# Performance work log

Hardware: AMD Instinct MI355X
Metric: run time of the kernel (lower is better)

The kernel has to match this reference:

```python
import jax, jax.numpy as jnp
import numpy as np

B, C, D, H, W = 4, 256, 16, 16, 16


def setup_inputs() -> dict:
    key = jax.random.key(0)
    ks = jax.random.split(key, 9)
    s = 1.0 / np.sqrt(C)
    inp = {
        "x": jax.random.normal(ks[0], (B, C, D, H, W), dtype=jnp.float32),
        "wq": jax.random.normal(ks[1], (C, C), dtype=jnp.float32) * s,
        "bq": jax.random.normal(ks[2], (C,), dtype=jnp.float32) * 0.02,
        "wk": jax.random.normal(ks[3], (C, C), dtype=jnp.float32) * s,
        "bk": jax.random.normal(ks[4], (C,), dtype=jnp.float32) * 0.02,
        "wv": jax.random.normal(ks[5], (C, C), dtype=jnp.float32) * s,
        "bv": jax.random.normal(ks[6], (C,), dtype=jnp.float32) * 0.02,
        "wp": jax.random.normal(ks[7], (C, C), dtype=jnp.float32) * s,
        "bp": jax.random.normal(ks[8], (C,), dtype=jnp.float32) * 0.02,
    }
    return inp


def reference(x, wq, bq, wk, bk, wv, bv, wp, bp):
    b, c, d, h, w = x.shape
    xf = x.reshape(b, c, d * h * w)  # (B, C, N)
    # 1x1 Conv3d == per-voxel linear map over channels
    q = jnp.einsum('oc,bcn->bon', wq, xf) + bq[:, None]
    k = jnp.einsum('oc,bcn->bon', wk, xf) + bk[:, None]
    v = jnp.einsum('oc,bcn->bon', wv, xf) + bv[:, None]
    # scores[b,i,j] = q[:, :, i] . k[:, :, j], scaled AFTER the bmm (as in source)
    scores = jnp.einsum('bci,bcj->bij', q, k) * (c ** -0.5)
    p = jax.nn.softmax(scores, axis=2)  # (B, N, N), softmax over keys j
    # attention[b,c,i] = sum_j v[b,c,j] * p[b,i,j]
    attn = jnp.einsum('bcj,bij->bci', v, p)
    out = jnp.einsum('oc,bcn->bon', wp, attn) + bp[:, None]
    return x + out.reshape(b, c, d, h, w)
```

## Files before the change

kernel.cpp:

```cpp
#include <hip/hip_runtime.h>

typedef unsigned short u16;
typedef unsigned int u32;
typedef __bf16 v8bf __attribute__((ext_vector_type(8)));
typedef float v4f __attribute__((ext_vector_type(4)));

#define DEV __device__ __forceinline__

constexpr int CB = 4;
constexpr int C = 256;
constexpr int NN = 4096;
constexpr float LOG2E = 1.4426950408889634f;
constexpr int PST = 44;

DEV u16 f2bf(float f) {
  union { float f; u32 u; } v; v.f = f;
  u32 r = v.u + 0x7fffu + ((v.u >> 16) & 1u);
  return (u16)(r >> 16);
}
DEV float bf2f(u16 h) {
  union { u32 u; float f; } v; v.u = ((u32)h) << 16; return v.f;
}

DEV void dma16(const u16* g, const u16* lds_base) {
  __builtin_amdgcn_global_load_lds(
      (const __attribute__((address_space(1))) void*)(unsigned long long)g,
      (__attribute__((address_space(3))) void*)(u32)(unsigned long long)lds_base,
      16, 0, 0);
}

__global__ __launch_bounds__(256) void k_transpose(const float* __restrict__ x,
                                                   u16* __restrict__ xT) {
  __shared__ float tile[32][33];
  int b = blockIdx.z;
  int n0 = blockIdx.x * 32, c0 = blockIdx.y * 32;
  int tx = threadIdx.x & 31, ty = threadIdx.x >> 5;
  const float* xb = x + (long)b * C * NN;
#pragma unroll
  for (int r = 0; r < 4; ++r)
    tile[ty + r * 8][tx] = xb[(long)(c0 + ty + r * 8) * NN + n0 + tx];
  __syncthreads();
  u16* xTb = xT + (long)b * NN * C;
#pragma unroll
  for (int r = 0; r < 4; ++r)
    xTb[(long)(n0 + ty + r * 8) * C + c0 + tx] = f2bf(tile[tx][ty + r * 8]);
}

__global__ __launch_bounds__(256) void k_cvt4(const float* __restrict__ s0,
                                              const float* __restrict__ s1,
                                              const float* __restrict__ s2,
                                              const float* __restrict__ s3,
                                              u16* __restrict__ d0, u16* __restrict__ d1,
                                              u16* __restrict__ d2, u16* __restrict__ d3,
                                              float* __restrict__ Mbuf) {
  if (blockIdx.x == 0 && blockIdx.y == 0 && threadIdx.x < 8) Mbuf[threadIdx.x] = 0.f;
  int wsel = blockIdx.y;
  const float* s = wsel == 0 ? s0 : wsel == 1 ? s1 : wsel == 2 ? s2 : s3;
  u16* d = wsel == 0 ? d0 : wsel == 1 ? d1 : wsel == 2 ? d2 : d3;
  int i = blockIdx.x * 256 + threadIdx.x;
  d[i] = f2bf(s[i]);
}

DEV void stage_dma(const u16* __restrict__ g, const u16* lds, int w, int lane) {
#pragma unroll
  for (int i = 0; i < 8; ++i) {
    int idx = w * 8 + i;
    int r = idx * 2 + (lane >> 5);
    int cg = (lane & 31) ^ (r & 7);
    dma16(g + (long)r * 256 + cg * 8, lds + idx * 512);
  }
}

__global__ __launch_bounds__(256) void k_qkv(
    const u16* __restrict__ xT, const u16* __restrict__ wqb, const u16* __restrict__ wkb,
    const u16* __restrict__ wvb, const float* __restrict__ bq, const float* __restrict__ bk,
    const float* __restrict__ bv, u16* __restrict__ qO, u16* __restrict__ kO,
    u16* __restrict__ vO, float* __restrict__ Pn) {
  __shared__ __align__(16) u16 Ash[64 * 256];
  __shared__ __align__(16) u16 Bsh[64 * 256];
  int t = threadIdx.x, w = t >> 6, lane = t & 63, lr = lane & 15, q = lane >> 4;
  int m0 = blockIdx.x * 64, n0 = blockIdx.y * 64, b = blockIdx.z;
  const int xk = lr & 7;
  stage_dma(xT + (long)b * NN * C + (long)m0 * 256, Ash, w, lane);
  stage_dma(wqb + (long)n0 * 256, Bsh, w, lane);
  asm volatile("s_waitcnt vmcnt(0)\n\ts_barrier" ::: "memory");
#pragma unroll 1
  for (int wsel = 0; wsel < 3; ++wsel) {
    v4f acc[4];
#pragma unroll
    for (int nt = 0; nt < 4; ++nt)
#pragma unroll
      for (int r = 0; r < 4; ++r) acc[nt][r] = 0.f;
#pragma unroll
    for (int ks = 0; ks < 8; ++ks) {
      int cg = ((ks * 4 + q) ^ xk) << 3;
      v8bf a = *reinterpret_cast<const v8bf*>(Ash + (w * 16 + lr) * 256 + cg);
#pragma unroll
      for (int nt = 0; nt < 4; ++nt) {
        v8bf bb = *reinterpret_cast<const v8bf*>(Bsh + (nt * 16 + lr) * 256 + cg);
        acc[nt] = __builtin_amdgcn_mfma_f32_16x16x32_bf16(a, bb, acc[nt], 0, 0, 0);
      }
    }
    asm volatile("s_waitcnt lgkmcnt(0)\n\ts_barrier" ::: "memory");
    if (wsel < 2) {
      stage_dma((wsel == 0 ? wkb : wvb) + (long)n0 * 256, Bsh, w, lane);
      const float* bias = wsel == 0 ? bq : bk;
      float sn[4] = {0.f, 0.f, 0.f, 0.f};
#pragma unroll
      for (int nt = 0; nt < 4; ++nt) {
#pragma unroll
        for (int r = 0; r < 4; ++r) {
          int gm = m0 + w * 16 + q * 4 + r;
          int gn = n0 + nt * 16 + lr;
          float val = acc[nt][r] + bias[gn];
          if (wsel == 0) {
            float vs = val * (0.0625f * LOG2E);
            qO[((long)b * NN + gm) * C + gn] = f2bf(vs);
            sn[r] += vs * vs;
          } else {
            kO[((long)b * NN + gm) * C + gn] = f2bf(val);
            sn[r] += val * val;
          }
        }
      }
#pragma unroll
      for (int r = 0; r < 4; ++r) {
#pragma unroll
        for (int d = 1; d < 16; d <<= 1) sn[r] += __shfl_xor(sn[r], d, 64);
      }
      if (lr == 0) {
#pragma unroll
        for (int r = 0; r < 4; ++r)
          Pn[(((long)wsel * 4 + blockIdx.y) * CB + b) * NN + m0 + w * 16 + q * 4 + r] =
              sn[r];
      }
      asm volatile("s_waitcnt vmcnt(0)\n\ts_barrier" ::: "memory");
    } else {
      u16* Vt = Ash;
#pragma unroll
      for (int nt = 0; nt < 4; ++nt) {
#pragma unroll
        for (int r = 0; r < 4; ++r) {
          int gn_l = nt * 16 + lr;
          int gm_l = w * 16 + q * 4 + r;
          float val = acc[nt][r] + bv[n0 + gn_l];
          Vt[gn_l * 72 + gm_l] = f2bf(val);
        }
      }
      asm volatile("s_waitcnt lgkmcnt(0)\n\ts_barrier" ::: "memory");
      int row = t >> 2;
      u16* vrow = vO + (long)b * C * NN + (long)(n0 + row) * NN + m0;
#pragma unroll
      for (int s2 = 0; s2 < 2; ++s2) {
        int seg = (t & 3) * 2 + s2;
        *reinterpret_cast<uint4*>(vrow + seg * 8) =
            *reinterpret_cast<const uint4*>(Vt + row * 72 + seg * 8);
      }
    }
  }
}

__global__ __launch_bounds__(256) void k_norm(const float* __restrict__ Pn,
                                              float* __restrict__ Mbuf) {
  int tsel = blockIdx.y, b = blockIdx.z;
  float mx = 0.f;
  for (int row = threadIdx.x; row < NN; row += 256) {
    float s = 0.f;
#pragma unroll
    for (int qr = 0; qr < 4; ++qr)
      s += Pn[(((long)tsel * 4 + qr) * CB + b) * NN + row];
    mx = fmaxf(mx, s);
  }
#pragma unroll
  for (int d = 1; d < 64; d <<= 1) mx = fmaxf(mx, __shfl_xor(mx, d, 64));
  if ((threadIdx.x & 63) == 0)
    atomicMax((u32*)(Mbuf + tsel * 4 + b), __float_as_uint(mx));
}

DEV void kissue(const u16* kb, const u16* kshb, int j0, int w, int lane) {
#pragma unroll
  for (int i = 0; i < 4; ++i) {
    int idx = w * 4 + i;
    int kr = idx * 2 + (lane >> 5);
    int kc = (lane & 31) ^ (kr & 7);
    dma16(kb + (long)(j0 + kr) * 256 + kc * 8, kshb + idx * 512);
  }
}

#define FLASH_STEP(IT, VL, VU, PW, PR, KC, KN)                                     \
  {                                                                                \
    int jn_ = ((IT) + 1 < niter) ? jstart + (((IT) + 1) << 5) : jstart;            \
    kissue(kb, (KN), jn_, w, lane);                                                \
    asm volatile("" ::: "memory");    \
    {                                                                              \
      int jv_ = jstart + ((IT) << 5);                                              \
      _Pragma("unroll") for (int cs = 0; cs < 4; ++cs)                             \
          VL[cs] = *reinterpret_cast<const v8bf*>(                                 \
              vbw + (long)(cs * 16 + lr) * NN + jv_ + q * 8);                      \
    }                                                                              \
    v4f s0a_, s0b_, s1a_, s1b_;                                                    \
    _Pragma("unroll") for (int r = 0; r < 4; ++r) {                                \
      s0a_[r] = 0.f; s0b_[r] = 0.f; s1a_[r] = 0.f; s1b_[r] = 0.f;                  \
    }                                                                              \
    __builtin_amdgcn_s_setprio(1);                                                 \
    _Pragma("unroll") for (int ks = 0; ks < 4; ++ks) {                             \
      int cgA_ = ((ks * 4 + q) ^ xk) << 3;                                         \
      int cgB_ = (((ks + 4) * 4 + q) ^ xk) << 3;                                   \
      v8bf k0a_ = *reinterpret_cast<const v8bf*>((KC) + lr * 256 + cgA_);          \
      v8bf k1a_ = *reinterpret_cast<const v8bf*>((KC) + (16 + lr) * 256 + cgA_);   \
      v8bf k0b_ = *reinterpret_cast<const v8bf*>((KC) + lr * 256 + cgB_);          \
      v8bf k1b_ = *reinterpret_cast<const v8bf*>((KC) + (16 + lr) * 256 + cgB_);   \
      s0a_ = __builtin_amdgcn_mfma_f32_16x16x32_bf16(qf[ks], k0a_, s0a_, 0, 0, 0); \
      s1a_ = __builtin_amdgcn_mfma_f32_16x16x32_bf16(qf[ks], k1a_, s1a_, 0, 0, 0); \
      s0b_ = __builtin_amdgcn_mfma_f32_16x16x32_bf16(qf[ks + 4], k0b_, s0b_, 0, 0, 0); \
      s1b_ = __builtin_amdgcn_mfma_f32_16x16x32_bf16(qf[ks + 4], k1b_, s1b_, 0, 0, 0); \
    }                                                                              \
    __builtin_amdgcn_s_setprio(0);                                                 \
    v4f s0_ = s0a_ + s0b_;                                                         \
    v4f s1_ = s1a_ + s1b_;                                                         \
    _Pragma("unroll") for (int r = 0; r < 4; ++r) {                                \
      float p0_ = exp2f(s0_[r] - M);                                               \
      float p1_ = exp2f(s1_[r] - M);                                               \
      lsum[r] += p0_ + p1_;                                                        \
      (PW)[(q * 4 + r) * PST + lr] = (u16)((__float_as_uint(p0_) + 0x8000u) >> 16);\
      (PW)[(q * 4 + r) * PST + 16 + lr] =                                          \
          (u16)((__float_as_uint(p1_) + 0x8000u) >> 16);                           \
    }                                                                              \
    if ((IT) > 0) {                                                                \
      v8bf pa_[4];                                                                 \
      _Pragma("unroll") for (int qs = 0; qs < 4; ++qs)                             \
          pa_[qs] = *reinterpret_cast<const v8bf*>(                                \
              (PR) + (qs * 16 + lr) * PST + q * 8);                                \
      __builtin_amdgcn_s_setprio(1);                                               \
      _Pragma("unroll") for (int cs = 0; cs < 4; ++cs)                             \
        _Pragma("unroll") for (int qs = 0; qs < 4; ++qs)                           \
          accO[qs * 4 + cs] = __builtin_amdgcn_mfma_f32_16x16x32_bf16(             \
              pa_[qs], VU[cs], accO[qs * 4 + cs], 0, 0, 0);                        \
      __builtin_amdgcn_s_setprio(0);                                               \
    }                                                                              \
    asm volatile("s_waitcnt vmcnt(4) lgkmcnt(0)\n\ts_barrier" ::: "memory");       \
  }

__global__ __launch_bounds__(256, 2) void k_flash(const u16* __restrict__ qT,
                                                  const u16* __restrict__ kT,
                                                  const u16* __restrict__ V,
                                                  u16* __restrict__ op0,
                                                  u16* __restrict__ op1,
                                                  float* __restrict__ ml,
                                                  const float* __restrict__ Mbuf,
                                                  int span) {
  __shared__ __align__(16) u16 ksh[2][32 * 256];
  __shared__ __align__(16) u16 psh[2][64 * PST];
  int t = threadIdx.x;
  int w = t >> 6, lane = t & 63, lr = lane & 15, q = lane >> 4;
  int total = gridDim.x * gridDim.y * gridDim.z;
  int flat = blockIdx.x + gridDim.x * (blockIdx.y + gridDim.y * blockIdx.z);
  int nf = (flat & 7) * (total >> 3) + (flat >> 3);
  int h = (nf >> 6) & (gridDim.y - 1);
  int b = nf >> (6 + __builtin_ctz(gridDim.y));
  int i0 = (nf & 63) * 64;
  const u16* qb = qT + ((long)b * NN + i0 + w * 16) * C;
  const u16* kb = kT + (long)b * NN * C;
  const u16* vbw = V + (long)b * C * NN + (long)(w * 64) * NN;
  float M = sqrtf(Mbuf[b] * Mbuf[4 + b]) + 1.5f;

  v8bf qf[8];
#pragma unroll
  for (int ks = 0; ks < 8; ++ks)
    qf[ks] = *reinterpret_cast<const v8bf*>(qb + lr * C + ks * 32 + q * 8);

  v4f accO[16];
#pragma unroll
  for (int ct = 0; ct < 16; ++ct)
#pragma unroll
    for (int r = 0; r < 4; ++r) accO[ct][r] = 0.f;
  float lsum[4] = {0.f, 0.f, 0.f, 0.f};

  u16* pw0 = psh[0] + w * 16 * PST;
  u16* pw1 = psh[1] + w * 16 * PST;
  const int xk = lr & 7;

  int jstart = h * span;
  int niter = span >> 5;

  kissue(kb, ksh[0], jstart, w, lane);
  asm volatile("s_waitcnt vmcnt(0)\n\ts_barrier" ::: "memory");

  v8bf vA[4] = {}, vB[4] = {};
#pragma unroll 1
  for (int it2 = 0; it2 < niter; it2 += 2) {
    FLASH_STEP(it2,     vA, vB, pw0, psh[1], ksh[0], ksh[1])
    FLASH_STEP(it2 + 1, vB, vA, pw1, psh[0], ksh[1], ksh[0])
  }
  {
    v8bf pa_[4];
#pragma unroll
    for (int qs = 0; qs < 4; ++qs)
      pa_[qs] = *reinterpret_cast<const v8bf*>(psh[1] + (qs * 16 + lr) * PST + q * 8);
#pragma unroll
    for (int cs = 0; cs < 4; ++cs)
#pragma unroll
      for (int qs = 0; qs < 4; ++qs)
        accO[qs * 4 + cs] = __builtin_amdgcn_mfma_f32_16x16x32_bf16(
            pa_[qs], vB[cs], accO[qs * 4 + cs], 0, 0, 0);
  }

#pragma unroll
  for (int r = 0; r < 4; ++r) {
#pragma unroll
    for (int d = 1; d < 16; d <<= 1) lsum[r] += __shfl_xor(lsum[r], d, 64);
  }
  u16* opp = h == 0 ? op0 : op1;
  u16* ob = opp + ((long)b * NN + i0) * C;
#pragma unroll
  for (int qs = 0; qs < 4; ++qs)
#pragma unroll
    for (int cs = 0; cs < 4; ++cs)
#pragma unroll
      for (int r = 0; r < 4; ++r)
        ob[(qs * 16 + q * 4 + r) * C + w * 64 + cs * 16 + lr] =
            f2bf(accO[qs * 4 + cs][r]);
  if (lr == 0) {
    long rbase = ((long)h * CB + b) * NN + i0 + w * 16 + q * 4;
#pragma unroll
    for (int r = 0; r < 4; ++r) {
      ml[(rbase + r) * 2] = M;
      ml[(rbase + r) * 2 + 1] = lsum[r];
    }
  }
}

__global__ __launch_bounds__(256) void k_gemmC(
    const u16* __restrict__ wpb, const u16* __restrict__ p0, const u16* __restrict__ p1,
    const float* __restrict__ ml, const float* __restrict__ bp,
    const float* __restrict__ x, float* __restrict__ out) {
  __shared__ __align__(16) u16 Ash[64 * 256];
  __shared__ __align__(16) u16 Bsh[64 * 256];
  int t = threadIdx.x;
  int w = t >> 6, lane = t & 63, lr = lane & 15, q = lane >> 4;
  int m0 = blockIdx.x * 64, n0 = blockIdx.y * 64, b = blockIdx.z;
  const int xk = lr & 7;
  const long nc = (long)NN * C;
  stage_dma(wpb + (long)m0 * 256, Ash, w, lane);
#pragma unroll
  for (int i = 0; i < 8; ++i) {
    int idx = w * 8 + i;
    int r = idx * 2 + (lane >> 5);
    int cg = (lane & 31) ^ (r & 7);
    long goff = (long)b * nc + (long)(n0 + r) * 256 + cg * 8;
    uint4 u0 = *reinterpret_cast<const uint4*>(p0 + goff);
    uint4 u1 = *reinterpret_cast<const uint4*>(p1 + goff);
    float l0 = ml[(((long)0 * CB + b) * NN + n0 + r) * 2 + 1];
    float l1 = ml[(((long)1 * CB + b) * NN + n0 + r) * 2 + 1];
    float inv = 1.0f / (l0 + l1);
    const u16* e0 = reinterpret_cast<const u16*>(&u0);
    const u16* e1 = reinterpret_cast<const u16*>(&u1);
    u16 cv[8];
#pragma unroll
    for (int k2 = 0; k2 < 8; ++k2)
      cv[k2] = f2bf((bf2f(e0[k2]) + bf2f(e1[k2])) * inv);
    *reinterpret_cast<uint4*>(Bsh + idx * 512 + lane * 8) =
        *reinterpret_cast<const uint4*>(cv);
  }
  asm volatile("s_waitcnt vmcnt(0) lgkmcnt(0)\n\ts_barrier" ::: "memory");
  v4f acc[4];
#pragma unroll
  for (int nt = 0; nt < 4; ++nt)
#pragma unroll
    for (int r = 0; r < 4; ++r) acc[nt][r] = 0.f;
#pragma unroll
  for (int ks = 0; ks < 8; ++ks) {
    int cg = ((ks * 4 + q) ^ xk) << 3;
    v8bf a = *reinterpret_cast<const v8bf*>(Ash + (w * 16 + lr) * 256 + cg);
#pragma unroll
    for (int nt = 0; nt < 4; ++nt) {
      v8bf bb = *reinterpret_cast<const v8bf*>(Bsh + (nt * 16 + lr) * 256 + cg);
      acc[nt] = __builtin_amdgcn_mfma_f32_16x16x32_bf16(a, bb, acc[nt], 0, 0, 0);
    }
  }
#pragma unroll
  for (int nt = 0; nt < 4; ++nt) {
#pragma unroll
    for (int r = 0; r < 4; ++r) {
      int gm = m0 + w * 16 + q * 4 + r;
      int gn = n0 + nt * 16 + lr;
      long addr = (long)b * nc + (long)gm * NN + gn;
      out[addr] = acc[nt][r] + bp[gm] + x[addr];
    }
  }
}

extern "C" void kernel_launch(void* const* d_in, const int* in_sizes, int n_in,
                              void* d_out, int out_size, void* d_ws, size_t ws_size,
                              hipStream_t stream) {
  const float* x = (const float*)d_in[0];
  const float* wq = (const float*)d_in[1];
  const float* bq = (const float*)d_in[2];
  const float* wk = (const float*)d_in[3];
  const float* bk = (const float*)d_in[4];
  const float* wv = (const float*)d_in[5];
  const float* bv = (const float*)d_in[6];
  const float* wp = (const float*)d_in[7];
  const float* bp = (const float*)d_in[8];
  float* out = (float*)d_out;
  char* ws = (char*)d_ws;

  const long SLOT = 8388608L;

  u16* wqb = (u16*)(ws + 0);
  u16* wkb = (u16*)(ws + 131072L);
  u16* wvb = (u16*)(ws + 262144L);
  u16* wpb = (u16*)(ws + 393216L);
  char* base = ws + 524288L;
  u16* xT  = (u16*)(base);
  u16* qTw = (u16*)(base + 1 * SLOT);
  u16* kTw = (u16*)(base + 2 * SLOT);
  u16* vw  = (u16*)(base + 3 * SLOT);
  u16* op1 = (u16*)(base + 4 * SLOT);
  float* ml = (float*)(base + 5 * SLOT);
  float* Mbuf = ml + 131072;
  u16* op0 = xT;
  float* Pn = (float*)op1;

  k_cvt4<<<dim3(256, 4), 256, 0, stream>>>(wq, wk, wv, wp, wqb, wkb, wvb, wpb, Mbuf);
  k_transpose<<<dim3(128, 8, CB), 256, 0, stream>>>(x, xT);
  k_qkv<<<dim3(64, 4, CB), 256, 0, stream>>>(xT, wqb, wkb, wvb, bq, bk, bv, qTw, kTw,
                                             vw, Pn);
  k_norm<<<dim3(1, 2, CB), 256, 0, stream>>>(Pn, Mbuf);
  k_flash<<<dim3(64, 2, CB), 256, 0, stream>>>(qTw, kTw, vw, op0, op1, ml, Mbuf,
                                               NN / 2);
  k_gemmC<<<dim3(4, 64, CB), 256, 0, stream>>>(wpb, op0, op1, ml, bp, x, out);
}
```

Baseline: 229.6 us.

## Fuse transpose and norm reduction into QKV kernel with double-buffered weights

Removes the separate x transpose/bf16 conversion kernel and the norm-max reduction kernel. The QKV kernel now loads fp32 x directly, transposes and converts it through LDS, then loops over all 12 weight tiles with double-buffered DMA staging. Row norms are reduced in-register and atomically maxed per block. This saves two launches and the xT round trip, but the grid shrinks from 1024 to 256 blocks, lowering parallelism. The V store also becomes an uncoalesced scalar transposed write.

```diff
diff --git a/kernel.cpp b/kernel.cpp
--- a/kernel.cpp
+++ b/kernel.cpp
@@ -27,23 +27,6 @@
       (const __attribute__((address_space(1))) void*)(unsigned long long)g,
       (__attribute__((address_space(3))) void*)(u32)(unsigned long long)lds_base,
       16, 0, 0);
-}
-
-__global__ __launch_bounds__(256) void k_transpose(const float* __restrict__ x,
-                                                   u16* __restrict__ xT) {
-  __shared__ float tile[32][33];
-  int b = blockIdx.z;
-  int n0 = blockIdx.x * 32, c0 = blockIdx.y * 32;
-  int tx = threadIdx.x & 31, ty = threadIdx.x >> 5;
-  const float* xb = x + (long)b * C * NN;
-#pragma unroll
-  for (int r = 0; r < 4; ++r)
-    tile[ty + r * 8][tx] = xb[(long)(c0 + ty + r * 8) * NN + n0 + tx];
-  __syncthreads();
-  u16* xTb = xT + (long)b * NN * C;
-#pragma unroll
-  for (int r = 0; r < 4; ++r)
-    xTb[(long)(n0 + ty + r * 8) * C + c0 + tx] = f2bf(tile[tx][ty + r * 8]);
 }
 
 __global__ __launch_bounds__(256) void k_cvt4(const float* __restrict__ s0,
@@ -72,20 +55,59 @@
 }
 
 __global__ __launch_bounds__(256) void k_qkv(
-    const u16* __restrict__ xT, const u16* __restrict__ wqb, const u16* __restrict__ wkb,
-    const u16* __restrict__ wvb, const float* __restrict__ bq, const float* __restrict__ bk,
+    const float* __restrict__ x, const u16* __restrict__ wqb,
+    const u16* __restrict__ wkb, const u16* __restrict__ wvb,
+    const float* __restrict__ bq, const float* __restrict__ bk,
     const float* __restrict__ bv, u16* __restrict__ qO, u16* __restrict__ kO,
-    u16* __restrict__ vO, float* __restrict__ Pn) {
+    u16* __restrict__ vO, float* __restrict__ Mbuf) {
   __shared__ __align__(16) u16 Ash[64 * 256];
-  __shared__ __align__(16) u16 Bsh[64 * 256];
+  __shared__ __align__(16) u16 Bsh[2][64 * 256];
   int t = threadIdx.x, w = t >> 6, lane = t & 63, lr = lane & 15, q = lane >> 4;
-  int m0 = blockIdx.x * 64, n0 = blockIdx.y * 64, b = blockIdx.z;
+  int m0 = blockIdx.x * 64, b = blockIdx.z;
   const int xk = lr & 7;
-  stage_dma(xT + (long)b * NN * C + (long)m0 * 256, Ash, w, lane);
-  stage_dma(wqb + (long)n0 * 256, Bsh, w, lane);
-  asm volatile("s_waitcnt vmcnt(0)\n\ts_barrier" ::: "memory");
+
+  {
+    float* scr = (float*)Bsh;
 #pragma unroll 1
-  for (int wsel = 0; wsel < 3; ++wsel) {
+    for (int cc = 0; cc < 4; ++cc) {
+#pragma unroll
+      for (int p = 0; p < 4; ++p) {
+        int cl = p * 16 + (t >> 4);
+        int nl = (t & 15) * 4;
+        *reinterpret_cast<float4*>(&scr[cl * 65 + nl]) =
+            *reinterpret_cast<const float4*>(
+                &x[((long)b * C + cc * 64 + cl) * NN + m0 + nl]);
+      }
+      __syncthreads();
+      int n = t >> 2;
+      int c0l = (t & 3) * 16;
+#pragma unroll
+      for (int j = 0; j < 2; ++j) {
+        u16 tmp[8];
+#pragma unroll
+        for (int e = 0; e < 8; ++e) tmp[e] = f2bf(scr[(c0l + j * 8 + e) * 65 + n]);
+        int cg = (cc * 8 + (t & 3) * 2 + j) ^ (n & 7);
+        *reinterpret_cast<uint4*>(&Ash[n * 256 + cg * 8]) =
+            *reinterpret_cast<const uint4*>(tmp);
+      }
+      __syncthreads();
+    }
+  }
+
+  stage_dma(wqb, Bsh[0], w, lane);
+  float sn[4] = {0.f, 0.f, 0.f, 0.f};
+#pragma unroll 1
+  for (int s = 0; s < 12; ++s) {
+    int wsel = s >> 2, n0q = s & 3;
+    const u16* cur = Bsh[s & 1];
+    if (s < 11) {
+      int s1 = s + 1;
+      const u16* wptr = (s1 >> 2) == 0 ? wqb : (s1 >> 2) == 1 ? wkb : wvb;
+      stage_dma(wptr + (long)((s1 & 3) * 64) * 256, Bsh[s1 & 1], w, lane);
+      asm volatile("s_waitcnt vmcnt(8)\n\ts_barrier" ::: "memory");
+    } else {
+      asm volatile("s_waitcnt vmcnt(0)\n\ts_barrier" ::: "memory");
+    }
     v4f acc[4];
 #pragma unroll
     for (int nt = 0; nt < 4; ++nt)
@@ -97,21 +119,18 @@
       v8bf a = *reinterpret_cast<const v8bf*>(Ash + (w * 16 + lr) * 256 + cg);
 #pragma unroll
       for (int nt = 0; nt < 4; ++nt) {
-        v8bf bb = *reinterpret_cast<const v8bf*>(Bsh + (nt * 16 + lr) * 256 + cg);
+        v8bf bb = *reinterpret_cast<const v8bf*>(cur + (nt * 16 + lr) * 256 + cg);
         acc[nt] = __builtin_amdgcn_mfma_f32_16x16x32_bf16(a, bb, acc[nt], 0, 0, 0);
       }
     }
-    asm volatile("s_waitcnt lgkmcnt(0)\n\ts_barrier" ::: "memory");
     if (wsel < 2) {
-      stage_dma((wsel == 0 ? wkb : wvb) + (long)n0 * 256, Bsh, w, lane);
       const float* bias = wsel == 0 ? bq : bk;
-      float sn[4] = {0.f, 0.f, 0.f, 0.f};
 #pragma unroll
       for (int nt = 0; nt < 4; ++nt) {
 #pragma unroll
         for (int r = 0; r < 4; ++r) {
           int gm = m0 + w * 16 + q * 4 + r;
-          int gn = n0 + nt * 16 + lr;
+          int gn = n0q * 64 + nt * 16 + lr;
           float val = acc[nt][r] + bias[gn];
           if (wsel == 0) {
             float vs = val * (0.0625f * LOG2E);
@@ -123,58 +142,33 @@
           }
         }
       }
-#pragma unroll
-      for (int r = 0; r < 4; ++r) {
-#pragma unroll
-        for (int d = 1; d < 16; d <<= 1) sn[r] += __shfl_xor(sn[r], d, 64);
-      }
-      if (lr == 0) {
-#pragma unroll
-        for (int r = 0; r < 4; ++r)
-          Pn[(((long)wsel * 4 + blockIdx.y) * CB + b) * NN + m0 + w * 16 + q * 4 + r] =
-              sn[r];
-      }
-      asm volatile("s_waitcnt vmcnt(0)\n\ts_barrier" ::: "memory");
+      if (n0q == 3) {
+#pragma unroll
+        for (int r = 0; r < 4; ++r) {
+#pragma unroll
+          for (int d = 1; d < 16; d <<= 1) sn[r] += __shfl_xor(sn[r], d, 64);
+        }
+        float mx = fmaxf(fmaxf(sn[0], sn[1]), fmaxf(sn[2], sn[3]));
+        mx = fmaxf(mx, __shfl_xor(mx, 16, 64));
+        mx = fmaxf(mx, __shfl_xor(mx, 32, 64));
+        if (lane == 0)
+          atomicMax((u32*)(Mbuf + wsel * 4 + b), __float_as_uint(mx));
+#pragma unroll
+        for (int r = 0; r < 4; ++r) sn[r] = 0.f;
+      }
     } else {
-      u16* Vt = Ash;
 #pragma unroll
       for (int nt = 0; nt < 4; ++nt) {
 #pragma unroll
         for (int r = 0; r < 4; ++r) {
-          int gn_l = nt * 16 + lr;
-          int gm_l = w * 16 + q * 4 + r;
-          float val = acc[nt][r] + bv[n0 + gn_l];
-          Vt[gn_l * 72 + gm_l] = f2bf(val);
+          int gn = n0q * 64 + nt * 16 + lr;
+          int gm = m0 + w * 16 + q * 4 + r;
+          vO[(long)b * C * NN + (long)gn * NN + gm] = f2bf(acc[nt][r] + bv[gn]);
         }
       }
-      asm volatile("s_waitcnt lgkmcnt(0)\n\ts_barrier" ::: "memory");
-      int row = t >> 2;
-      u16* vrow = vO + (long)b * C * NN + (long)(n0 + row) * NN + m0;
-#pragma unroll
-      for (int s2 = 0; s2 < 2; ++s2) {
-        int seg = (t & 3) * 2 + s2;
-        *reinterpret_cast<uint4*>(vrow + seg * 8) =
-            *reinterpret_cast<const uint4*>(Vt + row * 72 + seg * 8);
-      }
-    }
-  }
-}
-
-__global__ __launch_bounds__(256) void k_norm(const float* __restrict__ Pn,
-                                              float* __restrict__ Mbuf) {
-  int tsel = blockIdx.y, b = blockIdx.z;
-  float mx = 0.f;
-  for (int row = threadIdx.x; row < NN; row += 256) {
-    float s = 0.f;
-#pragma unroll
-    for (int qr = 0; qr < 4; ++qr)
-      s += Pn[(((long)tsel * 4 + qr) * CB + b) * NN + row];
-    mx = fmaxf(mx, s);
-  }
-#pragma unroll
-  for (int d = 1; d < 64; d <<= 1) mx = fmaxf(mx, __shfl_xor(mx, d, 64));
-  if ((threadIdx.x & 63) == 0)
-    atomicMax((u32*)(Mbuf + tsel * 4 + b), __float_as_uint(mx));
+    }
+    asm volatile("s_waitcnt lgkmcnt(0)\n\ts_barrier" ::: "memory");
+  }
 }
 
 DEV void kissue(const u16* kb, const u16* kshb, int j0, int w, int lane) {
@@ -412,21 +406,17 @@
   u16* wvb = (u16*)(ws + 262144L);
   u16* wpb = (u16*)(ws + 393216L);
   char* base = ws + 524288L;
-  u16* xT  = (u16*)(base);
+  u16* op0 = (u16*)(base);
   u16* qTw = (u16*)(base + 1 * SLOT);
   u16* kTw = (u16*)(base + 2 * SLOT);
   u16* vw  = (u16*)(base + 3 * SLOT);
   u16* op1 = (u16*)(base + 4 * SLOT);
   float* ml = (float*)(base + 5 * SLOT);
   float* Mbuf = ml + 131072;
-  u16* op0 = xT;
-  float* Pn = (float*)op1;
 
   k_cvt4<<<dim3(256, 4), 256, 0, stream>>>(wq, wk, wv, wp, wqb, wkb, wvb, wpb, Mbuf);
-  k_transpose<<<dim3(128, 8, CB), 256, 0, stream>>>(x, xT);
-  k_qkv<<<dim3(64, 4, CB), 256, 0, stream>>>(xT, wqb, wkb, wvb, bq, bk, bv, qTw, kTw,
-                                             vw, Pn);
-  k_norm<<<dim3(1, 2, CB), 256, 0, stream>>>(Pn, Mbuf);
+  k_qkv<<<dim3(64, 1, CB), 256, 0, stream>>>(x, wqb, wkb, wvb, bq, bk, bv, qTw, kTw,
+                                             vw, Mbuf);
   k_flash<<<dim3(64, 2, CB), 256, 0, stream>>>(qTw, kTw, vw, op0, op1, ml, Mbuf,
                                                NN / 2);
   k_gemmC<<<dim3(4, 64, CB), 256, 0, stream>>>(wpb, op0, op1, ml, bp, x, out);
```

Result: slower. 246.8 us (+7.5%).
